# Kernel tuning notes

Hardware: AMD Instinct MI355X
Metric: run time of the kernel (lower is better)

The kernel has to match this reference:

```python
import jax, jax.numpy as jnp
import numpy as np

N = 10000   # nodes
E = 160000  # edges per layer (avg degree 16)
B = 8       # batch of time windows
CIN = 32
S = 32      # spatial_channels
COUT = 32
NEG_SLOPE = 0.01  # F.leaky_relu default


def _xavier(k, shape):
    bound = np.sqrt(6.0 / (shape[0] + shape[1])).astype(np.float32)
    return jax.random.uniform(k, shape, jnp.float32, -bound, bound)


def setup_inputs() -> dict:
    key = jax.random.key(0)
    ks = jax.random.split(key, 20)
    return {
        "X": jax.random.normal(ks[0], (B, N, CIN), jnp.float32),
        "edge_index0": jax.random.randint(ks[1], (2, E), 0, N, jnp.int32),
        "edge_index1": jax.random.randint(ks[2], (2, E), 0, N, jnp.int32),
        "edge_weight0": jax.random.uniform(ks[3], (E,), jnp.float32),
        "edge_weight1": jax.random.uniform(ks[4], (E,), jnp.float32),
        "res_n_id0": jnp.arange(N, dtype=jnp.int32),
        "res_n_id1": jnp.arange(N, dtype=jnp.int32),
        # layer 1 params
        "Wn1": _xavier(ks[5], (CIN, S)),
        "We1": _xavier(ks[6], (1, S)),
        "Q1": _xavier(ks[7], (S, S)),
        "K1": _xavier(ks[8], (S, S)),
        "att_w1": _xavier(ks[9], (3 * S, 1)),
        "att_b1": jnp.zeros((1,), jnp.float32),
        "out_w1": _xavier(ks[10], (2 * S, S)),
        "out_b1": jnp.zeros((S,), jnp.float32),
        # layer 2 params
        "Wn2": _xavier(ks[11], (S, COUT)),
        "We2": _xavier(ks[12], (1, COUT)),
        "Q2": _xavier(ks[13], (COUT, COUT)),
        "K2": _xavier(ks[14], (COUT, COUT)),
        "att_w2": _xavier(ks[15], (3 * COUT, 1)),
        "att_b2": jnp.zeros((1,), jnp.float32),
        "out_w2": _xavier(ks[16], (2 * COUT, COUT)),
        "out_b2": jnp.zeros((COUT,), jnp.float32),
    }


def _egnn_conv(x_src, x_dst, edge_index, edge_w, Wn, We, Q, K, att_w, att_b, out_w, out_b):
    # x_src: [Ns, B, Cin], x_dst: [Nd, B, Cin], edge_index: [2, E], edge_w: [E]
    xs = x_src @ Wn                              # [Ns, B, O]
    xd = x_dst @ Wn                              # [Nd, B, O]
    ee = edge_w[:, None] @ We                    # [E, O]  (edge_channels = 1)
    src, dst = edge_index[0], edge_index[1]
    xj = xs[src]                                 # [E, B, O] gather source feats
    xi = xd[dst]                                 # [E, B, O] gather target feats
    q = xj @ Q                                   # [E, B, O]
    k = xi @ K                                   # [E, B, O]
    eb = jnp.broadcast_to(ee[:, None, :], q.shape)  # [E, B, O]
    att_feature = jnp.concatenate([q, k, eb], axis=-1)          # [E, B, 3O]
    att = jax.nn.sigmoid(att_feature @ att_w + att_b)           # [E, B, 1]
    msg = att * xj * jax.nn.sigmoid(eb)                         # [E, B, O]
    aggr = jnp.zeros_like(xd).at[dst].add(msg)                  # scatter-add -> [Nd, B, O]
    upd = jnp.concatenate([xd, aggr], axis=-1) @ out_w + out_b  # [Nd, B, O]
    return xd + upd


def reference(X, edge_index0, edge_index1, edge_weight0, edge_weight1,
              res_n_id0, res_n_id1,
              Wn1, We1, Q1, K1, att_w1, att_b1, out_w1, out_b1,
              Wn2, We2, Q2, K2, att_w2, att_b2, out_w2, out_b2):
    h = jnp.transpose(X, (1, 0, 2))              # [N, B, CIN]
    h = _egnn_conv(h, h[res_n_id0], edge_index0, edge_weight0,
                   Wn1, We1, Q1, K1, att_w1, att_b1, out_w1, out_b1)
    h = jax.nn.leaky_relu(h, NEG_SLOPE)
    h = _egnn_conv(h, h[res_n_id1], edge_index1, edge_weight1,
                   Wn2, We2, Q2, K2, att_w2, att_b2, out_w2, out_b2)
    h = jax.nn.leaky_relu(h, NEG_SLOPE)
    return jnp.transpose(h, (1, 0, 2))           # [B, N, COUT]
```

## Files before the change

### kernel.cpp

```cpp
#include <hip/hip_runtime.h>

#define NNODES 10000
#define NEDGES 160000
#define NB 8
#define NC 32
#define NCP 36
#define CAP 96
#define LUTB 2048
#define EBLKS 625
#define LUTBLKS 128
#define NWAVES 4000
#define GW 1000
#define KNODES 3
constexpr float NEG_SLOPE = 0.01f;

__device__ __forceinline__ float sigmoidf_(float x) {
    return 1.0f / (1.0f + __expf(-x));
}

__device__ __forceinline__ unsigned pk2bf(float a, float b) {
    unsigned ua = __float_as_uint(a);
    ua = (ua + 0x7fffu + ((ua >> 16) & 1u)) >> 16;
    unsigned ub = __float_as_uint(b);
    ub = (ub + 0x7fffu + ((ub >> 16) & 1u)) & 0xffff0000u;
    return ua | ub;
}

__global__ __launch_bounds__(256) void prologue_kernel(
    const float* Q1, const float* K1, const float* aw1, const float* We1,
    const float* Q2, const float* K2, const float* aw2, const float* We2,
    const int* __restrict__ ei0, const float* __restrict__ ew0,
    const float* __restrict__ ab1,
    float* consts, uint2* __restrict__ lut,
    int2* __restrict__ pkw1,
    int* __restrict__ cnt,
    unsigned* __restrict__ xs1h, unsigned* __restrict__ xs2h,
    float* __restrict__ sq1, float* __restrict__ sk1,
    const float* __restrict__ X, const float* __restrict__ Wn)
{
    int bx = blockIdx.x;
    int t = threadIdx.x;

    if (bx < EBLKS) {
        __shared__ float sCE, sAB;
        int e = bx * 256 + t;
        int src = ei0[e];
        int dst = ei0[NEDGES + e];
        float w = ew0[e];
        if (t < 32) {
            float p = We1[t] * aw1[64 + t];
            #pragma unroll
            for (int m = 16; m >= 1; m >>= 1) p += __shfl_xor(p, m, 32);
            if (t == 0) { sCE = p; sAB = ab1[0]; }
        }
        __syncthreads();
        int pos = atomicAdd(&cnt[dst], 1);
        if (pos < CAP) {
            int ix = (int)(w * (float)LUTB);
            ix = min(max(ix, 0), LUTB - 1);
            pkw1[(size_t)dst * CAP + pos] =
                make_int2(src | (ix << 14), __float_as_int(w * sCE + sAB));
        }
        return;
    }
    if (bx < EBLKS + LUTBLKS) {
        int i = (bx - EBLKS) * 256 + t;
        int layer = i >> 14;
        int bin   = (i >> 3) & (LUTB - 1);
        int o4    = i & 7;
        float w   = (bin + 0.5f) * (1.0f / LUTB);
        const float* We = layer ? We2 : We1;
        float s0 = sigmoidf_(w * We[o4 * 4 + 0]);
        float s1 = sigmoidf_(w * We[o4 * 4 + 1]);
        float s2 = sigmoidf_(w * We[o4 * 4 + 2]);
        float s3 = sigmoidf_(w * We[o4 * 4 + 3]);
        lut[i] = make_uint2(pk2bf(s0, s1), pk2bf(s2, s3));
        if (i < 128) {
            xs1h[(size_t)NNODES * 128 + i] = 0u;
            xs2h[(size_t)NNODES * 128 + i] = 0u;
        }
        return;
    }
    if (bx == EBLKS + LUTBLKS) {
        if (t < 32) {
            float aq2 = 0.f, ak2 = 0.f;
            for (int s = 0; s < 32; ++s) {
                aq2 += Q2[t * 32 + s] * aw2[s];
                ak2 += K2[t * 32 + s] * aw2[32 + s];
            }
            consts[64 + t] = aq2;
            consts[96 + t] = ak2;
        }
        return;
    }

    __shared__ float wnL[NC * NC];
    __shared__ float aqL[NC], akL[NC];
    __shared__ float xrow[4][NB][NC + 4];
    int w = t >> 6, l = t & 63, b = l >> 3, o4 = l & 7;
    int n = (bx - (EBLKS + LUTBLKS + 1)) * 4 + w;
    for (int i = t; i < NC * NC; i += 256) wnL[i] = Wn[i];
    if (t < 64) {
        int which = t >> 5, o = t & 31;
        const float* M  = which ? K1 : Q1;
        const float* av = aw1 + which * 32;
        float s = 0.f;
        for (int k = 0; k < 32; ++k) s += M[o * 32 + k] * av[k];
        (which ? akL : aqL)[o] = s;
    }
    const float4* X4 = (const float4*)X;
    float4 xv = X4[((size_t)b * NNODES + n) * 8 + o4];
    ((float4*)&xrow[w][b][0])[o4] = xv;
    __syncthreads();
    float4 aq = ((const float4*)aqL)[o4];
    float4 ak = ((const float4*)akL)[o4];
    const float4* wnL4 = (const float4*)wnL;
    float4 acc = {0.f, 0.f, 0.f, 0.f};
    #pragma unroll
    for (int c = 0; c < NC; ++c) {
        float xc = xrow[w][b][c];
        float4 w4 = wnL4[c * 8 + o4];
        acc.x += xc * w4.x; acc.y += xc * w4.y;
        acc.z += xc * w4.z; acc.w += xc * w4.w;
    }
    ((uint2*)xs1h)[(size_t)n * 64 + l] = make_uint2(pk2bf(acc.x, acc.y), pk2bf(acc.z, acc.w));
    float vq = acc.x * aq.x + acc.y * aq.y + acc.z * aq.z + acc.w * aq.w;
    float vk = acc.x * ak.x + acc.y * ak.y + acc.z * ak.z + acc.w * ak.w;
    #pragma unroll
    for (int m = 4; m >= 1; m >>= 1) {
        vq += __shfl_xor(vq, m);
        vk += __shfl_xor(vk, m);
    }
    if (o4 == 0) {
        sq1[n * NB + b] = vq;
        sk1[n * NB + b] = vk;
    }
}

template <int MODE>
__global__ __launch_bounds__(256) void gather_kernel(
    const int* __restrict__ cnt, const int2* __restrict__ pkw,
    const unsigned* __restrict__ xsh,
    const float* __restrict__ sq, const float* __restrict__ sk,
    const uint2* __restrict__ luth,
    const float* __restrict__ consts,
    const float* __restrict__ ow, const float* __restrict__ ob,
    const float* __restrict__ Wn2,
    unsigned* __restrict__ xs2h, float* __restrict__ sq2, float* __restrict__ sk2,
    float* __restrict__ outp,
    const int* __restrict__ ei1, const float* __restrict__ ew1,
    const float* __restrict__ ab2, const float* __restrict__ aw2,
    const float* __restrict__ We2,
    int* __restrict__ cnt2, int2* __restrict__ pkw2)
{
    int t = threadIdx.x;

    if (MODE == 0 && blockIdx.x >= GW) {
        __shared__ float sCE, sAB;
        int e = (blockIdx.x - GW) * 256 + t;
        int src = ei1[e];
        int dst = ei1[NEDGES + e];
        float w = ew1[e];
        if (t < 32) {
            float p = We2[t] * aw2[64 + t];
            #pragma unroll
            for (int m = 16; m >= 1; m >>= 1) p += __shfl_xor(p, m, 32);
            if (t == 0) { sCE = p; sAB = ab2[0]; }
        }
        __syncthreads();
        int pos = atomicAdd(&cnt2[dst], 1);
        if (pos < CAP) {
            int ix = (int)(w * (float)LUTB);
            ix = min(max(ix, 0), LUTB - 1);
            pkw2[(size_t)dst * CAP + pos] =
                make_int2(src | (ix << 14), __float_as_int(w * sCE + sAB));
        }
        return;
    }

    __shared__ __align__(16) float owL[2 * NC * NC];
    __shared__ __align__(16) float wnL[(MODE == 0) ? NC * NC : 4];
    __shared__ __align__(16) float xL[4][NB][NCP];
    __shared__ __align__(16) float aL[4][NB][NCP];

    int w = t >> 6, l = t & 63, b = l >> 3, o4 = l & 7;
    int wid = blockIdx.x * 4 + w;
    for (int i = t; i < 2 * NC * NC; i += 256) owL[i] = ow[i];
    if (MODE == 0)
        for (int i = t; i < NC * NC; i += 256) wnL[i] = Wn2[i];
    __syncthreads();

    const float4* owL4 = (const float4*)owL;
    const float4* wnL4 = (const float4*)wnL;
    const uint2*  XH   = (const uint2*)xsh;

    int degA = cnt[wid];
    const int2* ppA = pkw + (size_t)wid * CAP;
    int2  mcA  = ppA[o4];
    float skbA = sk[wid * NB + b];
    float sqA  = sq[(mcA.x & 16383) * NB + b];

    for (int k = 0; k < KNODES; ++k) {
        int n = wid + k * NWAVES;
        if (n >= NNODES) break;
        int nn = wid + (k + 1) * NWAVES;
        bool hasN = (k + 1 < KNODES) && (nn < NNODES);

        int degB = 0; int2 mcB = make_int2((int)NNODES, 0); float skbB = 0.f;
        const int2* ppB = pkw;
        if (hasN) {
            degB = cnt[nn];
            ppB  = pkw + (size_t)nn * CAP;
            mcB  = ppB[o4];
            skbB = sk[nn * NB + b];
        }

        int deg = min(degA, CAP - 24);
        float4 acc = {0.f, 0.f, 0.f, 0.f};
        int2 mc = mcA; float sqc = sqA;
        for (int c0 = 0; c0 < deg; c0 += 8) {
            int2 mn = ppA[c0 + 8 + o4];
            float sqn = sq[(mn.x & 16383) * NB + b];
            float att_own = (c0 + o4 < deg)
                          ? sigmoidf_(sqc + skbA + __int_as_float(mc.y)) : 0.f;
            #pragma unroll
            for (int j = 0; j < 8; ++j) {
                int spk = __builtin_amdgcn_readlane(mc.x, j);
                int ssrc, six;
                if (c0 + j < deg) {
                    ssrc = spk & 16383;
                    six  = (spk >> 14) & 2047;
                } else {
                    ssrc = NNODES;
                    six  = 0;
                }
                uint2 hx = XH[(size_t)ssrc * 64 + l];
                uint2 hg = luth[six * 8 + o4];
                float at = __shfl(att_own, b * 8 + j);
                acc.x += at * __uint_as_float(hg.x << 16)          * __uint_as_float(hx.x << 16);
                acc.y += at * __uint_as_float(hg.x & 0xffff0000u)  * __uint_as_float(hx.x & 0xffff0000u);
                acc.z += at * __uint_as_float(hg.y << 16)          * __uint_as_float(hx.y << 16);
                acc.w += at * __uint_as_float(hg.y & 0xffff0000u)  * __uint_as_float(hx.y & 0xffff0000u);
            }
            mc = mn; sqc = sqn;
        }

        float sqB = 0.f;
        if (hasN) sqB = sq[(mcB.x & 16383) * NB + b];

        uint2 hv = XH[(size_t)n * 64 + l];
        float4 xv;
        xv.x = __uint_as_float(hv.x << 16);
        xv.y = __uint_as_float(hv.x & 0xffff0000u);
        xv.z = __uint_as_float(hv.y << 16);
        xv.w = __uint_as_float(hv.y & 0xffff0000u);
        ((float4*)&xL[w][b][0])[o4] = xv;
        ((float4*)&aL[w][b][0])[o4] = acc;
        float4 u = ((const float4*)ob)[o4];
        #pragma unroll 4
        for (int c = 0; c < NC; ++c) {
            float xc = xL[w][b][c];
            float ac = aL[w][b][c];
            float4 w1 = owL4[c * 8 + o4];
            float4 w2 = owL4[(NC + c) * 8 + o4];
            u.x += xc * w1.x + ac * w2.x;
            u.y += xc * w1.y + ac * w2.y;
            u.z += xc * w1.z + ac * w2.z;
            u.w += xc * w1.w + ac * w2.w;
        }
        float4 r;
        r.x = xv.x + u.x; r.y = xv.y + u.y; r.z = xv.z + u.z; r.w = xv.w + u.w;
        r.x = (r.x > 0.f) ? r.x : NEG_SLOPE * r.x;
        r.y = (r.y > 0.f) ? r.y : NEG_SLOPE * r.y;
        r.z = (r.z > 0.f) ? r.z : NEG_SLOPE * r.z;
        r.w = (r.w > 0.f) ? r.w : NEG_SLOPE * r.w;

        if (MODE == 1) {
            ((float4*)outp)[((size_t)b * NNODES + n) * 8 + o4] = r;
        } else {
            ((float4*)&xL[w][b][0])[o4] = r;
            float4 a2 = {0.f, 0.f, 0.f, 0.f};
            #pragma unroll 4
            for (int c = 0; c < NC; ++c) {
                float hc = xL[w][b][c];
                float4 w0 = wnL4[c * 8 + o4];
                a2.x += hc * w0.x;
                a2.y += hc * w0.y;
                a2.z += hc * w0.z;
                a2.w += hc * w0.w;
            }
            ((uint2*)xs2h)[(size_t)n * 64 + l] = make_uint2(pk2bf(a2.x, a2.y), pk2bf(a2.z, a2.w));
            float4 aqv = ((const float4*)(consts + 64))[o4];
            float4 akv = ((const float4*)(consts + 96))[o4];
            float vq = a2.x*aqv.x + a2.y*aqv.y + a2.z*aqv.z + a2.w*aqv.w;
            float vk = a2.x*akv.x + a2.y*akv.y + a2.z*akv.z + a2.w*akv.w;
            #pragma unroll
            for (int m = 4; m >= 1; m >>= 1) {
                vq += __shfl_xor(vq, m);
                vk += __shfl_xor(vk, m);
            }
            if (o4 == 0) {
                sq2[n * NB + b] = vq;
                sk2[n * NB + b] = vk;
            }
        }

        degA = degB; ppA = ppB; mcA = mcB; skbA = skbB; sqA = sqB;
    }
}

extern "C" void kernel_launch(void* const* d_in, const int* in_sizes, int n_in,
                              void* d_out, int out_size, void* d_ws, size_t ws_size,
                              hipStream_t stream) {
    const float* X    = (const float*)d_in[0];
    const int*   ei0  = (const int*)  d_in[1];
    const int*   ei1  = (const int*)  d_in[2];
    const float* ew0  = (const float*)d_in[3];
    const float* ew1  = (const float*)d_in[4];
    const float* Wn1  = (const float*)d_in[7];
    const float* We1  = (const float*)d_in[8];
    const float* Q1   = (const float*)d_in[9];
    const float* K1   = (const float*)d_in[10];
    const float* aw1  = (const float*)d_in[11];
    const float* ab1  = (const float*)d_in[12];
    const float* ow1  = (const float*)d_in[13];
    const float* ob1  = (const float*)d_in[14];
    const float* Wn2  = (const float*)d_in[15];
    const float* We2  = (const float*)d_in[16];
    const float* Q2   = (const float*)d_in[17];
    const float* K2   = (const float*)d_in[18];
    const float* aw2  = (const float*)d_in[19];
    const float* ab2  = (const float*)d_in[20];
    const float* ow2  = (const float*)d_in[21];
    const float* ob2  = (const float*)d_in[22];

    const size_t ROWH = (size_t)(NNODES + 1) * 128;
    const size_t SS   = (size_t)(NNODES + 1) * NB;
    unsigned* XS1H  = (unsigned*)d_ws;
    unsigned* XS2H  = XS1H + ROWH;
    float* SQ1    = (float*)(XS2H + ROWH);
    float* SK1    = SQ1 + SS;
    float* SQ2    = SK1 + SS;
    float* SK2    = SQ2 + SS;
    float* CONSTS = SK2 + SS;
    uint2* LUTH   = (uint2*)(CONSTS + 160);
    int*   CNT    = (int*)(LUTH + 2 * LUTB * 8);
    int2*  PKW1   = (int2*)(CNT + 2 * NNODES);
    int2*  PKW2   = PKW1 + (size_t)NNODES * CAP;

    hipMemsetAsync(CNT, 0, 2 * NNODES * sizeof(int), stream);
    prologue_kernel<<<EBLKS + LUTBLKS + 1 + NNODES / 4, 256, 0, stream>>>(
        Q1, K1, aw1, We1, Q2, K2, aw2, We2, ei0, ew0, ab1,
        CONSTS, LUTH, PKW1, CNT, XS1H, XS2H, SQ1, SK1, X, Wn1);

    gather_kernel<0><<<GW + EBLKS, 256, 0, stream>>>(
        CNT, PKW1, XS1H, SQ1, SK1, LUTH, CONSTS,
        ow1, ob1, Wn2, XS2H, SQ2, SK2, nullptr,
        ei1, ew1, ab2, aw2, We2, CNT + NNODES, PKW2);
    gather_kernel<1><<<GW, 256, 0, stream>>>(
        CNT + NNODES, PKW2, XS2H, SQ2, SK2, LUTH + LUTB * 8, CONSTS,
        ow2, ob2, nullptr, nullptr, nullptr, nullptr, (float*)d_out,
        nullptr, nullptr, nullptr, nullptr, nullptr, nullptr, nullptr);
}
```

Baseline: 87.45 us.

## Split each node's batch dimension across two blocks to double gather parallelism

Each destination node's eight batch slices are now divided between two blocks (four batches each), so grid width doubles and each lane handles two channels instead of four. Neighbor feature and LUT loads become 32-bit per lane, and the output/projection math uses float2 with a wider shuffle reduction. This is meant to raise occupancy and memory-level parallelism in the latency-bound gather. In exchange, edge lists, attention sigmoids and weight loads into shared memory are duplicated across the two halves.

```diff
diff --git a/kernel.cpp b/kernel.cpp
--- a/kernel.cpp
+++ b/kernel.cpp
@@ -10,7 +10,7 @@
 #define EBLKS 625
 #define LUTBLKS 128
 #define NWAVES 4000
-#define GW 1000
+#define GW 2000
 #define KNODES 3
 constexpr float NEG_SLOPE = 0.01f;
 
@@ -142,7 +142,7 @@
     const int* __restrict__ cnt, const int2* __restrict__ pkw,
     const unsigned* __restrict__ xsh,
     const float* __restrict__ sq, const float* __restrict__ sk,
-    const uint2* __restrict__ luth,
+    const unsigned* __restrict__ luth,
     const float* __restrict__ consts,
     const float* __restrict__ ow, const float* __restrict__ ob,
     const float* __restrict__ Wn2,
@@ -180,25 +180,33 @@
 
     __shared__ __align__(16) float owL[2 * NC * NC];
     __shared__ __align__(16) float wnL[(MODE == 0) ? NC * NC : 4];
-    __shared__ __align__(16) float xL[4][NB][NCP];
-    __shared__ __align__(16) float aL[4][NB][NCP];
-
-    int w = t >> 6, l = t & 63, b = l >> 3, o4 = l & 7;
-    int wid = blockIdx.x * 4 + w;
+    __shared__ __align__(16) float xL[4][4][NCP];
+    __shared__ __align__(16) float aL[4][4][NCP];
+
+    int bx = blockIdx.x;
+    int w = t >> 6, l = t & 63;
+    int half = (bx >> 2) & 1;
+    int gq   = ((bx >> 3) << 2) | (bx & 3);
+    int wid  = gq * 4 + w;
+    int ba   = l >> 4;
+    int o16  = l & 15;
+    int la   = l & 31;
+    int jown = la & 7;
+    int bown = half * 4 + ((la >> 3) & 3);
+
     for (int i = t; i < 2 * NC * NC; i += 256) owL[i] = ow[i];
     if (MODE == 0)
         for (int i = t; i < NC * NC; i += 256) wnL[i] = Wn2[i];
     __syncthreads();
 
-    const float4* owL4 = (const float4*)owL;
-    const float4* wnL4 = (const float4*)wnL;
-    const uint2*  XH   = (const uint2*)xsh;
+    const float2* owL2 = (const float2*)owL;
+    const float2* wnL2 = (const float2*)wnL;
 
     int degA = cnt[wid];
     const int2* ppA = pkw + (size_t)wid * CAP;
-    int2  mcA  = ppA[o4];
-    float skbA = sk[wid * NB + b];
-    float sqA  = sq[(mcA.x & 16383) * NB + b];
+    int2  mcA  = ppA[jown];
+    float skbA = sk[wid * NB + bown];
+    float sqA  = sq[(mcA.x & 16383) * NB + bown];
 
     for (int k = 0; k < KNODES; ++k) {
         int n = wid + k * NWAVES;
@@ -211,17 +219,17 @@
         if (hasN) {
             degB = cnt[nn];
             ppB  = pkw + (size_t)nn * CAP;
-            mcB  = ppB[o4];
-            skbB = sk[nn * NB + b];
+            mcB  = ppB[jown];
+            skbB = sk[nn * NB + bown];
         }
 
         int deg = min(degA, CAP - 24);
-        float4 acc = {0.f, 0.f, 0.f, 0.f};
+        float2 acc = {0.f, 0.f};
         int2 mc = mcA; float sqc = sqA;
         for (int c0 = 0; c0 < deg; c0 += 8) {
-            int2 mn = ppA[c0 + 8 + o4];
-            float sqn = sq[(mn.x & 16383) * NB + b];
-            float att_own = (c0 + o4 < deg)
+            int2 mn = ppA[c0 + 8 + jown];
+            float sqn = sq[(mn.x & 16383) * NB + bown];
+            float att_own = (c0 + jown < deg)
                           ? sigmoidf_(sqc + skbA + __int_as_float(mc.y)) : 0.f;
             #pragma unroll
             for (int j = 0; j < 8; ++j) {
@@ -234,72 +242,63 @@
                     ssrc = NNODES;
                     six  = 0;
                 }
-                uint2 hx = XH[(size_t)ssrc * 64 + l];
-                uint2 hg = luth[six * 8 + o4];
-                float at = __shfl(att_own, b * 8 + j);
-                acc.x += at * __uint_as_float(hg.x << 16)          * __uint_as_float(hx.x << 16);
-                acc.y += at * __uint_as_float(hg.x & 0xffff0000u)  * __uint_as_float(hx.x & 0xffff0000u);
-                acc.z += at * __uint_as_float(hg.y << 16)          * __uint_as_float(hx.y << 16);
-                acc.w += at * __uint_as_float(hg.y & 0xffff0000u)  * __uint_as_float(hx.y & 0xffff0000u);
+                unsigned hx = xsh[(size_t)ssrc * 128 + half * 64 + l];
+                unsigned hg = luth[six * 16 + o16];
+                float at = __shfl(att_own, ba * 8 + j);
+                acc.x += at * __uint_as_float(hg << 16)          * __uint_as_float(hx << 16);
+                acc.y += at * __uint_as_float(hg & 0xffff0000u)  * __uint_as_float(hx & 0xffff0000u);
             }
             mc = mn; sqc = sqn;
         }
 
         float sqB = 0.f;
-        if (hasN) sqB = sq[(mcB.x & 16383) * NB + b];
-
-        uint2 hv = XH[(size_t)n * 64 + l];
-        float4 xv;
-        xv.x = __uint_as_float(hv.x << 16);
-        xv.y = __uint_as_float(hv.x & 0xffff0000u);
-        xv.z = __uint_as_float(hv.y << 16);
-        xv.w = __uint_as_float(hv.y & 0xffff0000u);
-        ((float4*)&xL[w][b][0])[o4] = xv;
-        ((float4*)&aL[w][b][0])[o4] = acc;
-        float4 u = ((const float4*)ob)[o4];
+        if (hasN) sqB = sq[(mcB.x & 16383) * NB + bown];
+
+        unsigned hv = xsh[(size_t)n * 128 + half * 64 + l];
+        float2 xv;
+        xv.x = __uint_as_float(hv << 16);
+        xv.y = __uint_as_float(hv & 0xffff0000u);
+        ((float2*)&xL[w][ba][0])[o16] = xv;
+        ((float2*)&aL[w][ba][0])[o16] = acc;
+        float2 u = ((const float2*)ob)[o16];
         #pragma unroll 4
         for (int c = 0; c < NC; ++c) {
-            float xc = xL[w][b][c];
-            float ac = aL[w][b][c];
-            float4 w1 = owL4[c * 8 + o4];
-            float4 w2 = owL4[(NC + c) * 8 + o4];
+            float xc = xL[w][ba][c];
+            float ac = aL[w][ba][c];
+            float2 w1 = owL2[c * 16 + o16];
+            float2 w2 = owL2[(NC + c) * 16 + o16];
             u.x += xc * w1.x + ac * w2.x;
             u.y += xc * w1.y + ac * w2.y;
-            u.z += xc * w1.z + ac * w2.z;
-            u.w += xc * w1.w + ac * w2.w;
-        }
-        float4 r;
-        r.x = xv.x + u.x; r.y = xv.y + u.y; r.z = xv.z + u.z; r.w = xv.w + u.w;
+        }
+        float2 r;
+        r.x = xv.x + u.x; r.y = xv.y + u.y;
         r.x = (r.x > 0.f) ? r.x : NEG_SLOPE * r.x;
         r.y = (r.y > 0.f) ? r.y : NEG_SLOPE * r.y;
-        r.z = (r.z > 0.f) ? r.z : NEG_SLOPE * r.z;
-        r.w = (r.w > 0.f) ? r.w : NEG_SLOPE * r.w;
-
+
+        int b = half * 4 + ba;
         if (MODE == 1) {
-            ((float4*)outp)[((size_t)b * NNODES + n) * 8 + o4] = r;
+            ((float2*)outp)[((size_t)b * NNODES + n) * 16 + o16] = r;
         } else {
-            ((float4*)&xL[w][b][0])[o4] = r;
-            float4 a2 = {0.f, 0.f, 0.f, 0.f};
+            ((float2*)&xL[w][ba][0])[o16] = r;
+            float2 a2 = {0.f, 0.f};
             #pragma unroll 4
             for (int c = 0; c < NC; ++c) {
-                float hc = xL[w][b][c];
-                float4 w0 = wnL4[c * 8 + o4];
+                float hc = xL[w][ba][c];
+                float2 w0 = wnL2[c * 16 + o16];
                 a2.x += hc * w0.x;
                 a2.y += hc * w0.y;
-                a2.z += hc * w0.z;
-                a2.w += hc * w0.w;
-            }
-            ((uint2*)xs2h)[(size_t)n * 64 + l] = make_uint2(pk2bf(a2.x, a2.y), pk2bf(a2.z, a2.w));
-            float4 aqv = ((const float4*)(consts + 64))[o4];
-            float4 akv = ((const float4*)(consts + 96))[o4];
-            float vq = a2.x*aqv.x + a2.y*aqv.y + a2.z*aqv.z + a2.w*aqv.w;
-            float vk = a2.x*akv.x + a2.y*akv.y + a2.z*akv.z + a2.w*akv.w;
+            }
+            xs2h[(size_t)n * 128 + half * 64 + l] = pk2bf(a2.x, a2.y);
+            float2 aqv = ((const float2*)(consts + 64))[o16];
+            float2 akv = ((const float2*)(consts + 96))[o16];
+            float vq = a2.x * aqv.x + a2.y * aqv.y;
+            float vk = a2.x * akv.x + a2.y * akv.y;
             #pragma unroll
-            for (int m = 4; m >= 1; m >>= 1) {
+            for (int m = 8; m >= 1; m >>= 1) {
                 vq += __shfl_xor(vq, m);
                 vk += __shfl_xor(vk, m);
             }
-            if (o4 == 0) {
+            if (o16 == 0) {
                 sq2[n * NB + b] = vq;
                 sk2[n * NB + b] = vk;
             }
@@ -354,11 +353,11 @@
         CONSTS, LUTH, PKW1, CNT, XS1H, XS2H, SQ1, SK1, X, Wn1);
 
     gather_kernel<0><<<GW + EBLKS, 256, 0, stream>>>(
-        CNT, PKW1, XS1H, SQ1, SK1, LUTH, CONSTS,
+        CNT, PKW1, XS1H, SQ1, SK1, (const unsigned*)LUTH, CONSTS,
         ow1, ob1, Wn2, XS2H, SQ2, SK2, nullptr,
         ei1, ew1, ab2, aw2, We2, CNT + NNODES, PKW2);
     gather_kernel<1><<<GW, 256, 0, stream>>>(
-        CNT + NNODES, PKW2, XS2H, SQ2, SK2, LUTH + LUTB * 8, CONSTS,
+        CNT + NNODES, PKW2, XS2H, SQ2, SK2, (const unsigned*)(LUTH + LUTB * 8), CONSTS,
         ow2, ob2, nullptr, nullptr, nullptr, nullptr, (float*)d_out,
         nullptr, nullptr, nullptr, nullptr, nullptr, nullptr, nullptr);
 }
```

Result: slower. 106.3 us (+21.5%).
